# Kernel tuning notes

Hardware: AMD Instinct MI355X
Metric: run time of the kernel (lower is better)

Reference implementation:

```python
import jax, jax.numpy as jnp
import numpy as np


def setup_inputs() -> dict:
    key = jax.random.key(0)
    k1, k2, k3 = jax.random.split(key, 3)
    B, C, H, W = 4, 3, 1024, 1024
    NUM_CLASSES = 8
    x = jax.random.uniform(k1, (B, C, H, W), dtype=jnp.float32)
    y = jax.random.uniform(k2, (B, C, H, W), dtype=jnp.float32)
    mask_y = jax.random.normal(k3, (B, NUM_CLASSES, H, W), dtype=jnp.float32)
    return {"x": x, "y": y, "mask_y": mask_y}


def reference(x, y, mask_y):
    # Per-label segment loss: for each segmentation label, build the masked
    # region of the channel-averaged image, fill the outside with the region
    # mean, and accumulate three consistency losses.
    num_classes = mask_y.shape[1]
    mask_arg = jnp.argmax(mask_y, axis=1, keepdims=True)  # [B,1,H,W] int labels
    x_avg = jnp.mean(x, axis=1, keepdims=True)            # [B,1,H,W]
    y_avg = jnp.mean(y, axis=1, keepdims=True)            # [B,1,H,W]

    def per_label(label):
        m = (mask_arg == label)
        x_region = jnp.where(m, x_avg, 0.0)
        x_region_avg = jnp.mean(x_region)                 # mean over full tensor
        x_region = jnp.where(x_region == 0.0, x_region_avg, x_region)
        y_region = jnp.where(m, y_avg, 0.0)
        y_region_avg = jnp.mean(y_region)
        y_region = jnp.where(y_region == 0.0, y_region_avg, y_region)
        loss1 = jnp.mean(x_region ** y_region)
        loss2 = x_region_avg ** y_region_avg
        loss3 = jnp.mean((x_region - x_region_avg) ** 2)
        return loss1, loss2, loss3

    l1, l2, l3 = jax.vmap(per_label)(jnp.arange(num_classes))
    return (jnp.sum(l1), jnp.sum(l2), jnp.sum(l3))
```

## Files before the change

kernel.cpp:

```cpp
#include <hip/hip_runtime.h>
#include <math.h>

#define HW_     (1024 * 1024)
#define NPIX    (4 * HW_)
#define NG      (NPIX / 4)
#define NSETS   64
#define ACC_STRIDE 32
#define BLOCK_  256
#define GRID1   (NG / BLOCK_)

__device__ __forceinline__ float fast_pow_pos(float x, float p) {
    return __builtin_amdgcn_exp2f(p * __builtin_amdgcn_logf(x));
}

__global__ __launch_bounds__(BLOCK_, 4) void pass1_kernel(
    const float* __restrict__ x, const float* __restrict__ y,
    const float* __restrict__ mk, double* __restrict__ acc)
{
    const int g  = blockIdx.x * BLOCK_ + threadIdx.x;
    const int p0 = g << 2;
    const int b  = p0 >> 20;
    const int hw = p0 & (HW_ - 1);

    const size_t xb = (size_t)(b * 3) * HW_ + hw;
    const size_t mb = (size_t)(b * 8) * HW_ + hw;

    const float4 x0 = *(const float4*)(x + xb);
    const float4 x1 = *(const float4*)(x + xb + HW_);
    const float4 x2 = *(const float4*)(x + xb + 2 * (size_t)HW_);
    const float4 y0 = *(const float4*)(y + xb);
    const float4 y1 = *(const float4*)(y + xb + HW_);
    const float4 y2 = *(const float4*)(y + xb + 2 * (size_t)HW_);
    const float4 m0 = *(const float4*)(mk + mb);
    const float4 m1 = *(const float4*)(mk + mb + 1 * (size_t)HW_);
    const float4 m2 = *(const float4*)(mk + mb + 2 * (size_t)HW_);
    const float4 m3 = *(const float4*)(mk + mb + 3 * (size_t)HW_);
    const float4 m4 = *(const float4*)(mk + mb + 4 * (size_t)HW_);
    const float4 m5 = *(const float4*)(mk + mb + 5 * (size_t)HW_);
    const float4 m6 = *(const float4*)(mk + mb + 6 * (size_t)HW_);
    const float4 m7 = *(const float4*)(mk + mb + 7 * (size_t)HW_);

    __builtin_amdgcn_sched_barrier(0);

    float sx[8], sy[8], sc[8];
#pragma unroll
    for (int l = 0; l < 8; ++l) { sx[l] = 0.f; sy[l] = 0.f; sc[l] = 0.f; }
    float spw = 0.f, sxx = 0.f;

    const float inv3 = 1.0f / 3.0f;

#define PIX(F)                                                              \
    {                                                                       \
        const float xav = (x0.F + x1.F + x2.F) * inv3;                      \
        const float yav = (y0.F + y1.F + y2.F) * inv3;                      \
        float best = m0.F; int bi = 0;                                      \
        if (m1.F > best) { best = m1.F; bi = 1; }                           \
        if (m2.F > best) { best = m2.F; bi = 2; }                           \
        if (m3.F > best) { best = m3.F; bi = 3; }                           \
        if (m4.F > best) { best = m4.F; bi = 4; }                           \
        if (m5.F > best) { best = m5.F; bi = 5; }                           \
        if (m6.F > best) { best = m6.F; bi = 6; }                           \
        if (m7.F > best) { best = m7.F; bi = 7; }                           \
        _Pragma("unroll")                                                   \
        for (int l = 0; l < 8; ++l) {                                       \
            const bool p = (bi == l);                                       \
            sx[l] += p ? xav : 0.0f;                                        \
            sy[l] += p ? yav : 0.0f;                                        \
            sc[l] += p ? 1.0f : 0.0f;                                       \
        }                                                                   \
        spw += fast_pow_pos(xav, yav);         \
        sxx += xav * xav;                                                   \
    }

    PIX(x) PIX(y) PIX(z) PIX(w)
#undef PIX

#pragma unroll
    for (int off = 32; off > 0; off >>= 1) {
#pragma unroll
        for (int l = 0; l < 8; ++l) {
            sx[l] += __shfl_down(sx[l], off);
            sy[l] += __shfl_down(sy[l], off);
            sc[l] += __shfl_down(sc[l], off);
        }
        spw += __shfl_down(spw, off);
        sxx += __shfl_down(sxx, off);
    }
    __shared__ float red[4][26];
    const int wave = threadIdx.x >> 6, lane = threadIdx.x & 63;
    if (lane == 0) {
#pragma unroll
        for (int l = 0; l < 8; ++l) {
            red[wave][l]      = sx[l];
            red[wave][8 + l]  = sy[l];
            red[wave][16 + l] = sc[l];
        }
        red[wave][24] = spw;
        red[wave][25] = sxx;
    }
    __syncthreads();
    if (threadIdx.x < 26) {
        float t = red[0][threadIdx.x] + red[1][threadIdx.x] +
                  red[2][threadIdx.x] + red[3][threadIdx.x];
        atomicAdd(&acc[(blockIdx.x & (NSETS - 1)) * ACC_STRIDE + threadIdx.x],
                  (double)t);
    }
}

__global__ void finalize_kernel(const double* __restrict__ acc,
                                float* __restrict__ out)
{
    __shared__ double sh[26];
    int t = threadIdx.x;
    if (t < 26) {
        double s = 0.0;
        for (int k = 0; k < NSETS; ++k) s += acc[k * ACC_STRIDE + t];
        sh[t] = s;
    }
    __syncthreads();
    if (t == 0) {
        const double invN = 1.0 / (double)NPIX;
        double l1 = sh[24];
        double l3 = sh[25];
        double l2 = 0.0;
        for (int l = 0; l < 8; ++l) {
            double SX  = sh[l];
            double XA  = SX * invN;
            double YA  = sh[8 + l] * invN;
            double cnt = sh[16 + l];
            double pw  = pow(XA, YA);
            l2 += pw;
            l1 += ((double)NPIX - cnt) * pw;
            l3 += cnt * XA * XA - 2.0 * XA * SX;
        }
        out[0] = (float)(l1 * invN);
        out[1] = (float)l2;
        out[2] = (float)(l3 * invN);
    }
}

extern "C" void kernel_launch(void* const* d_in, const int* in_sizes, int n_in,
                              void* d_out, int out_size, void* d_ws, size_t ws_size,
                              hipStream_t stream)
{
    const float* x  = (const float*)d_in[0];
    const float* y  = (const float*)d_in[1];
    const float* mk = (const float*)d_in[2];
    float* out = (float*)d_out;

    double* acc = (double*)d_ws;
    (void)hipMemsetAsync(acc, 0, NSETS * ACC_STRIDE * 8, stream);

    pass1_kernel<<<GRID1, BLOCK_, 0, stream>>>(x, y, mk, acc);
    finalize_kernel<<<1, 64, 0, stream>>>(acc, out);
}
```

Before: 269.5 us.

## Process four float4 runs per thread with streaming channel accumulation

Each thread now handles 16 pixels (4 strided float4 runs) instead of 4, so the grid shrinks fourfold. Channels are loaded and reduced in place (running sums for x/y, running argmax for the mask) in stages separated by sched barriers, which keeps register pressure bounded while issuing 4 loads per stage. The aim is to cut the per-block reduction and atomic overhead and keep more memory requests in flight per thread. In exchange there are fewer blocks to hide latency, and the barriers limit how freely the compiler can schedule.

```diff
diff --git a/kernel.cpp b/kernel.cpp
--- a/kernel.cpp
+++ b/kernel.cpp
@@ -7,7 +7,9 @@
 #define NSETS   64
 #define ACC_STRIDE 32
 #define BLOCK_  256
-#define GRID1   (NG / BLOCK_)
+#define TILE_G  1024
+#define RUN     4
+#define GRID1   (NG / TILE_G)
 
 __device__ __forceinline__ float fast_pow_pos(float x, float p) {
     return __builtin_amdgcn_exp2f(p * __builtin_amdgcn_logf(x));
@@ -17,53 +19,81 @@
     const float* __restrict__ x, const float* __restrict__ y,
     const float* __restrict__ mk, double* __restrict__ acc)
 {
-    const int g  = blockIdx.x * BLOCK_ + threadIdx.x;
-    const int p0 = g << 2;
-    const int b  = p0 >> 20;
-    const int hw = p0 & (HW_ - 1);
+    const int tid  = threadIdx.x;
+    const int wave = tid >> 6, lane = tid & 63;
+    const int t    = blockIdx.x;
+    const int b    = t >> 8;
+    const size_t hw0 = (size_t)(t & 255) * 4096 + (size_t)wave * 1024
+                     + (size_t)lane * 4;
 
-    const size_t xb = (size_t)(b * 3) * HW_ + hw;
-    const size_t mb = (size_t)(b * 8) * HW_ + hw;
+    const float* xp = x  + (size_t)(b * 3) * HW_ + hw0;
+    const float* yp = y  + (size_t)(b * 3) * HW_ + hw0;
+    const float* mp = mk + (size_t)(b * 8) * HW_ + hw0;
 
-    const float4 x0 = *(const float4*)(x + xb);
-    const float4 x1 = *(const float4*)(x + xb + HW_);
-    const float4 x2 = *(const float4*)(x + xb + 2 * (size_t)HW_);
-    const float4 y0 = *(const float4*)(y + xb);
-    const float4 y1 = *(const float4*)(y + xb + HW_);
-    const float4 y2 = *(const float4*)(y + xb + 2 * (size_t)HW_);
-    const float4 m0 = *(const float4*)(mk + mb);
-    const float4 m1 = *(const float4*)(mk + mb + 1 * (size_t)HW_);
-    const float4 m2 = *(const float4*)(mk + mb + 2 * (size_t)HW_);
-    const float4 m3 = *(const float4*)(mk + mb + 3 * (size_t)HW_);
-    const float4 m4 = *(const float4*)(mk + mb + 4 * (size_t)HW_);
-    const float4 m5 = *(const float4*)(mk + mb + 5 * (size_t)HW_);
-    const float4 m6 = *(const float4*)(mk + mb + 6 * (size_t)HW_);
-    const float4 m7 = *(const float4*)(mk + mb + 7 * (size_t)HW_);
+    float4 xs[RUN], ys[RUN];
+#pragma unroll
+    for (int r = 0; r < RUN; ++r) xs[r] = *(const float4*)(xp + r * 256);
+#pragma unroll
+    for (int c = 1; c < 3; ++c) {
+        __builtin_amdgcn_sched_barrier(0);
+#pragma unroll
+        for (int r = 0; r < RUN; ++r) {
+            const float4 v = *(const float4*)(xp + (size_t)c * HW_ + r * 256);
+            xs[r].x += v.x; xs[r].y += v.y; xs[r].z += v.z; xs[r].w += v.w;
+        }
+    }
+    __builtin_amdgcn_sched_barrier(0);
+#pragma unroll
+    for (int r = 0; r < RUN; ++r) ys[r] = *(const float4*)(yp + r * 256);
+#pragma unroll
+    for (int c = 1; c < 3; ++c) {
+        __builtin_amdgcn_sched_barrier(0);
+#pragma unroll
+        for (int r = 0; r < RUN; ++r) {
+            const float4 v = *(const float4*)(yp + (size_t)c * HW_ + r * 256);
+            ys[r].x += v.x; ys[r].y += v.y; ys[r].z += v.z; ys[r].w += v.w;
+        }
+    }
+    const float inv3 = 1.0f / 3.0f;
+#pragma unroll
+    for (int r = 0; r < RUN; ++r) {
+        xs[r].x *= inv3; xs[r].y *= inv3; xs[r].z *= inv3; xs[r].w *= inv3;
+        ys[r].x *= inv3; ys[r].y *= inv3; ys[r].z *= inv3; ys[r].w *= inv3;
+    }
 
+    float4 best[RUN]; int4 bi[RUN];
     __builtin_amdgcn_sched_barrier(0);
+#pragma unroll
+    for (int r = 0; r < RUN; ++r) {
+        best[r] = *(const float4*)(mp + r * 256);
+        bi[r].x = 0; bi[r].y = 0; bi[r].z = 0; bi[r].w = 0;
+    }
+#pragma unroll
+    for (int c = 1; c < 8; ++c) {
+        __builtin_amdgcn_sched_barrier(0);
+#pragma unroll
+        for (int r = 0; r < RUN; ++r) {
+            const float4 v = *(const float4*)(mp + (size_t)c * HW_ + r * 256);
+            if (v.x > best[r].x) { best[r].x = v.x; bi[r].x = c; }
+            if (v.y > best[r].y) { best[r].y = v.y; bi[r].y = c; }
+            if (v.z > best[r].z) { best[r].z = v.z; bi[r].z = c; }
+            if (v.w > best[r].w) { best[r].w = v.w; bi[r].w = c; }
+        }
+    }
 
     float sx[8], sy[8], sc[8];
 #pragma unroll
     for (int l = 0; l < 8; ++l) { sx[l] = 0.f; sy[l] = 0.f; sc[l] = 0.f; }
     float spw = 0.f, sxx = 0.f;
 
-    const float inv3 = 1.0f / 3.0f;
-
-#define PIX(F)                                                              \
+#define PIX(R, F)                                                           \
     {                                                                       \
-        const float xav = (x0.F + x1.F + x2.F) * inv3;                      \
-        const float yav = (y0.F + y1.F + y2.F) * inv3;                      \
-        float best = m0.F; int bi = 0;                                      \
-        if (m1.F > best) { best = m1.F; bi = 1; }                           \
-        if (m2.F > best) { best = m2.F; bi = 2; }                           \
-        if (m3.F > best) { best = m3.F; bi = 3; }                           \
-        if (m4.F > best) { best = m4.F; bi = 4; }                           \
-        if (m5.F > best) { best = m5.F; bi = 5; }                           \
-        if (m6.F > best) { best = m6.F; bi = 6; }                           \
-        if (m7.F > best) { best = m7.F; bi = 7; }                           \
+        const float xav = xs[R].F;                                          \
+        const float yav = ys[R].F;                                          \
+        const int   lab = bi[R].F;                                          \
         _Pragma("unroll")                                                   \
         for (int l = 0; l < 8; ++l) {                                       \
-            const bool p = (bi == l);                                       \
+            const bool p = (lab == l);                                      \
             sx[l] += p ? xav : 0.0f;                                        \
             sy[l] += p ? yav : 0.0f;                                        \
             sc[l] += p ? 1.0f : 0.0f;                                       \
@@ -72,7 +102,8 @@
         sxx += xav * xav;                                                   \
     }
 
-    PIX(x) PIX(y) PIX(z) PIX(w)
+#pragma unroll
+    for (int r = 0; r < RUN; ++r) { PIX(r, x) PIX(r, y) PIX(r, z) PIX(r, w) }
 #undef PIX
 
 #pragma unroll
@@ -87,7 +118,6 @@
         sxx += __shfl_down(sxx, off);
     }
     __shared__ float red[4][26];
-    const int wave = threadIdx.x >> 6, lane = threadIdx.x & 63;
     if (lane == 0) {
 #pragma unroll
         for (int l = 0; l < 8; ++l) {
@@ -99,11 +129,10 @@
         red[wave][25] = sxx;
     }
     __syncthreads();
-    if (threadIdx.x < 26) {
-        float t = red[0][threadIdx.x] + red[1][threadIdx.x] +
-                  red[2][threadIdx.x] + red[3][threadIdx.x];
-        atomicAdd(&acc[(blockIdx.x & (NSETS - 1)) * ACC_STRIDE + threadIdx.x],
-                  (double)t);
+    if (tid < 26) {
+        float s = red[0][tid] + red[1][tid] + red[2][tid] + red[3][tid];
+        atomicAdd(&acc[(blockIdx.x & (NSETS - 1)) * ACC_STRIDE + tid],
+                  (double)s);
     }
 }
 
```

New measurement: 265.6 us. About the same (-1.5%).
